# Kernel tuning notes

Measured on AMD Instinct MI355X. Metric: run time of the kernel, lower is better.

## Reference

```python
import jax, jax.numpy as jnp
import numpy as np

HIDDEN = 64
INPUT = 19


def _lstm_layer(x, Wih, Whh, bih, bhh):
    # x: [B, T, I]; Wih: [4H, I]; Whh: [4H, H]; biases: [4H]
    B, T, _ = x.shape
    H = Whh.shape[1]
    # Input contribution for all timesteps at once (big GEMM).
    zx = jnp.einsum('bti,gi->btg', x, Wih) + bih + bhh  # [B, T, 4H]

    def step(carry, z_t):
        h, c = carry
        z = z_t + h @ Whh.T  # [B, 4H]
        i, f, g, o = jnp.split(z, 4, axis=-1)  # torch gate order: i, f, g, o
        i = jax.nn.sigmoid(i)
        f = jax.nn.sigmoid(f)
        g = jnp.tanh(g)
        o = jax.nn.sigmoid(o)
        c = f * c + i * g
        h = o * jnp.tanh(c)
        return (h, c), h

    h0 = jnp.zeros((B, H), x.dtype)
    (_, _), hs = jax.lax.scan(step, (h0, h0), jnp.swapaxes(zx, 0, 1))
    return jnp.swapaxes(hs, 0, 1)  # [B, T, H]


def setup_inputs() -> dict:
    key = jax.random.key(0)
    ks = jax.random.split(key, 12)
    B, T = 4096, 168
    s = 1.0 / np.sqrt(HIDDEN)  # torch LSTM/Linear init scale
    u = lambda k, shape: jax.random.uniform(k, shape, jnp.float32, -s, s)
    return {
        'x': jax.random.normal(ks[0], (B, T, INPUT), jnp.float32),
        'Wih0': u(ks[1], (4 * HIDDEN, INPUT)),
        'Whh0': u(ks[2], (4 * HIDDEN, HIDDEN)),
        'bih0': u(ks[3], (4 * HIDDEN,)),
        'bhh0': u(ks[4], (4 * HIDDEN,)),
        'Wih1': u(ks[5], (4 * HIDDEN, HIDDEN)),
        'Whh1': u(ks[6], (4 * HIDDEN, HIDDEN)),
        'bih1': u(ks[7], (4 * HIDDEN,)),
        'bhh1': u(ks[8], (4 * HIDDEN,)),
        'Wfc': u(ks[9], (1, HIDDEN)),
        'bfc': u(ks[10], (1,)),
    }


def reference(x, Wih0, Whh0, bih0, bhh0, Wih1, Whh1, bih1, bhh1, Wfc, bfc):
    h1 = _lstm_layer(x, Wih0, Whh0, bih0, bhh0)   # [B, T, H]
    h2 = _lstm_layer(h1, Wih1, Whh1, bih1, bhh1)  # [B, T, H]
    out = h2[:, -1, :] @ Wfc.T + bfc              # [B, 1]
    return out.squeeze(-1)                        # [B]
```

## Files before the change

kernel.cpp:

```cpp
#include <hip/hip_runtime.h>
#include <math.h>

#define T_STEPS 168
#define INP     19
#define HID     64
#define ROWS    16
#define NTH     512
#define HSTH    72
#define XSTH    40

typedef _Float16 half8   __attribute__((ext_vector_type(8)));
typedef float    floatx4 __attribute__((ext_vector_type(4)));

__device__ __forceinline__ float fast_sigmoid(float x) {
    return __builtin_amdgcn_rcpf(1.0f + __expf(-x));
}
__device__ __forceinline__ float fast_tanh(float x) {
    return 1.0f - 2.0f * __builtin_amdgcn_rcpf(1.0f + __expf(2.0f * x));
}

__global__ __launch_bounds__(NTH) __attribute__((amdgpu_waves_per_eu(2, 2)))
void lstm2_mfma3_kernel(const float* __restrict__ x,
                        const float* __restrict__ Wih0, const float* __restrict__ Whh0,
                        const float* __restrict__ bih0, const float* __restrict__ bhh0,
                        const float* __restrict__ Wih1, const float* __restrict__ Whh1,
                        const float* __restrict__ bih1, const float* __restrict__ bhh1,
                        const float* __restrict__ Wfc,  const float* __restrict__ bfc,
                        float* __restrict__ out)
{
    __shared__ __align__(16) _Float16 xf [2][ROWS][XSTH];
    __shared__ __align__(16) _Float16 h1f[2][ROWS][HSTH];
    __shared__ __align__(16) _Float16 h2f[2][ROWS][HSTH];
    __shared__ float hout[ROWS][HID];

    const int tid  = threadIdx.x;
    const int b0   = blockIdx.x * ROWS;
    const int wv   = tid >> 6;
    const int lane = tid & 63;
    const int quad = lane >> 4;
    const int l16  = lane & 15;
    const int kq   = quad * 8;
    const int lay  = wv >> 2;
    const int uq   = wv & 3;
    const int u    = uq * 16 + l16;

    half8 bfr[4][4];
    float bz[4];
#pragma unroll
    for (int gi = 0; gi < 4; ++gi) {
        const int gr = gi * 64 + u;
        if (lay == 0) {
            const float* wr = Wih0 + gr * INP;
#pragma unroll
            for (int e = 0; e < 8; ++e) {
                const int k = kq + e;
                bfr[gi][0][e] = (k < INP) ? (_Float16)wr[k] : (_Float16)0.0f;
            }
            const float* hr = Whh0 + gr * HID;
#pragma unroll
            for (int e = 0; e < 8; ++e) {
                bfr[gi][1][e] = (_Float16)hr[kq + e];
                bfr[gi][2][e] = (_Float16)hr[32 + kq + e];
            }
            bfr[gi][3] = bfr[gi][2];
            bz[gi] = bih0[gr] + bhh0[gr];
        } else {
            const float* ir = Wih1 + gr * HID;
            const float* hr = Whh1 + gr * HID;
#pragma unroll
            for (int e = 0; e < 8; ++e) {
                bfr[gi][0][e] = (_Float16)ir[kq + e];
                bfr[gi][1][e] = (_Float16)ir[32 + kq + e];
                bfr[gi][2][e] = (_Float16)hr[kq + e];
                bfr[gi][3][e] = (_Float16)hr[32 + kq + e];
            }
            bz[gi] = bih1[gr] + bhh1[gr];
        }
    }

    float cst[4] = {0.f, 0.f, 0.f, 0.f};

    int srr = 0, sii = 0;
    const float* xsrc = nullptr;
    if (tid < ROWS * INP) {
        srr = tid / INP; sii = tid - srr * INP;
        xsrc = x + ((size_t)(b0 + srr) * T_STEPS) * INP + sii;
    }

    for (int e = tid; e < 2 * ROWS * XSTH; e += NTH) ((_Float16*)xf)[e] = (_Float16)0.f;
    for (int e = tid; e < 2 * ROWS * HSTH; e += NTH) {
        ((_Float16*)h1f)[e] = (_Float16)0.f;
        ((_Float16*)h2f)[e] = (_Float16)0.f;
    }
    __syncthreads();
    float xreg = 0.f;
    if (xsrc) {
        xf[0][srr][sii] = (_Float16)xsrc[0];
        xreg = xsrc[INP];
    }
    __syncthreads();

    for (int t = 0; t <= T_STEPS; ++t) {
        float xnew = 0.f;
        if (xsrc) {
            const int tn = (t + 2 < T_STEPS) ? (t + 2) : (T_STEPS - 1);
            xnew = xsrc[(size_t)tn * INP];
        }
        if (xsrc && (t + 1) < T_STEPS)
            xf[(t + 1) & 1][srr][sii] = (_Float16)xreg;

        const bool act = (lay == 0) ? (t < T_STEPS) : (t >= 1);
        if (act) {
            floatx4 acc[4];
#pragma unroll
            for (int gi = 0; gi < 4; ++gi)
                acc[gi] = (floatx4){bz[gi], bz[gi], bz[gi], bz[gi]};
            if (lay == 0) {
                const half8 ax = *(const half8*)&xf [t & 1][l16][kq];
                const half8 a0 = *(const half8*)&h1f[(t + 1) & 1][l16][kq];
                const half8 a1 = *(const half8*)&h1f[(t + 1) & 1][l16][32 + kq];
#pragma unroll
                for (int gi = 0; gi < 4; ++gi) {
                    acc[gi] = __builtin_amdgcn_mfma_f32_16x16x32_f16(ax, bfr[gi][0], acc[gi], 0, 0, 0);
                    acc[gi] = __builtin_amdgcn_mfma_f32_16x16x32_f16(a0, bfr[gi][1], acc[gi], 0, 0, 0);
                    acc[gi] = __builtin_amdgcn_mfma_f32_16x16x32_f16(a1, bfr[gi][2], acc[gi], 0, 0, 0);
                }
            } else {
                const half8 p0 = *(const half8*)&h1f[(t + 1) & 1][l16][kq];
                const half8 p1 = *(const half8*)&h1f[(t + 1) & 1][l16][32 + kq];
                const half8 q0 = *(const half8*)&h2f[t & 1][l16][kq];
                const half8 q1 = *(const half8*)&h2f[t & 1][l16][32 + kq];
#pragma unroll
                for (int gi = 0; gi < 4; ++gi) {
                    acc[gi] = __builtin_amdgcn_mfma_f32_16x16x32_f16(p0, bfr[gi][0], acc[gi], 0, 0, 0);
                    acc[gi] = __builtin_amdgcn_mfma_f32_16x16x32_f16(p1, bfr[gi][1], acc[gi], 0, 0, 0);
                    acc[gi] = __builtin_amdgcn_mfma_f32_16x16x32_f16(q0, bfr[gi][2], acc[gi], 0, 0, 0);
                    acc[gi] = __builtin_amdgcn_mfma_f32_16x16x32_f16(q1, bfr[gi][3], acc[gi], 0, 0, 0);
                }
            }
#pragma unroll
            for (int rg = 0; rg < 4; ++rg) {
                const float ig = fast_sigmoid(acc[0][rg]);
                const float fg = fast_sigmoid(acc[1][rg]);
                const float gg = fast_tanh(acc[2][rg]);
                const float og = fast_sigmoid(acc[3][rg]);
                cst[rg] = fg * cst[rg] + ig * gg;
                const float hv = og * fast_tanh(cst[rg]);
                const int row = quad * 4 + rg;
                if (lay == 0) {
                    h1f[t & 1][row][u] = (_Float16)hv;
                } else {
                    h2f[(t + 1) & 1][row][u] = (_Float16)hv;
                    if (t == T_STEPS) hout[row][u] = hv;
                }
            }
        }
        xreg = xnew;
        __syncthreads();
    }

    if (tid < ROWS) {
        float a = bfc[0];
        const float* hr = hout[tid];
#pragma unroll
        for (int k = 0; k < HID; ++k)
            a = fmaf(hr[k], Wfc[k], a);
        out[b0 + tid] = a;
    }
}

extern "C" void kernel_launch(void* const* d_in, const int* in_sizes, int n_in,
                              void* d_out, int out_size, void* d_ws, size_t ws_size,
                              hipStream_t stream) {
    const float* x    = (const float*)d_in[0];
    const float* Wih0 = (const float*)d_in[1];
    const float* Whh0 = (const float*)d_in[2];
    const float* bih0 = (const float*)d_in[3];
    const float* bhh0 = (const float*)d_in[4];
    const float* Wih1 = (const float*)d_in[5];
    const float* Whh1 = (const float*)d_in[6];
    const float* bih1 = (const float*)d_in[7];
    const float* bhh1 = (const float*)d_in[8];
    const float* Wfc  = (const float*)d_in[9];
    const float* bfc  = (const float*)d_in[10];
    float* out = (float*)d_out;

    const int B = in_sizes[0] / (T_STEPS * INP);
    const int grid = B / ROWS;

    lstm2_mfma3_kernel<<<dim3(grid), dim3(NTH), 0, stream>>>(
        x, Wih0, Whh0, bih0, bhh0, Wih1, Whh1, bih1, bhh1, Wfc, bfc, out);
}
```

Baseline: 254.5 us.

## Double waves per block to split gate activations and fold exp scaling into weights

```diff
diff --git a/kernel.cpp b/kernel.cpp
--- a/kernel.cpp
+++ b/kernel.cpp
@@ -5,22 +5,28 @@
 #define INP     19
 #define HID     64
 #define ROWS    16
-#define NTH     512
+#define NTH     1024
 #define HSTH    72
 #define XSTH    40
 
 typedef _Float16 half8   __attribute__((ext_vector_type(8)));
 typedef float    floatx4 __attribute__((ext_vector_type(4)));
 
-__device__ __forceinline__ float fast_sigmoid(float x) {
-    return __builtin_amdgcn_rcpf(1.0f + __expf(-x));
-}
-__device__ __forceinline__ float fast_tanh(float x) {
-    return 1.0f - 2.0f * __builtin_amdgcn_rcpf(1.0f + __expf(2.0f * x));
-}
-
-__global__ __launch_bounds__(NTH) __attribute__((amdgpu_waves_per_eu(2, 2)))
-void lstm2_mfma3_kernel(const float* __restrict__ x,
+#define KSIG  (-1.4426950408889634f)
+#define KTANH ( 2.8853900817779268f)
+
+__device__ __forceinline__ float exp2_hw(float x) {
+    float r; asm("v_exp_f32 %0, %1" : "=v"(r) : "v"(x)); return r;
+}
+__device__ __forceinline__ float sig_pre(float a) {
+    return __builtin_amdgcn_rcpf(1.0f + exp2_hw(a));
+}
+__device__ __forceinline__ float tanh_pre(float a) {
+    return 1.0f - 2.0f * __builtin_amdgcn_rcpf(1.0f + exp2_hw(a));
+}
+
+__global__ __launch_bounds__(NTH) __attribute__((amdgpu_waves_per_eu(4, 4)))
+void lstm2_mfma4_kernel(const float* __restrict__ x,
                         const float* __restrict__ Wih0, const float* __restrict__ Whh0,
                         const float* __restrict__ bih0, const float* __restrict__ bhh0,
                         const float* __restrict__ Wih1, const float* __restrict__ Whh1,
@@ -40,7 +46,8 @@
     const int quad = lane >> 4;
     const int l16  = lane & 15;
     const int kq   = quad * 8;
-    const int lay  = wv >> 2;
+    const int lay  = wv >> 3;
+    const int sub  = (wv >> 2) & 1;
     const int uq   = wv & 3;
     const int u    = uq * 16 + l16;
 
@@ -48,37 +55,38 @@
     float bz[4];
 #pragma unroll
     for (int gi = 0; gi < 4; ++gi) {
+        const float sc = (gi == 2) ? KTANH : KSIG;
         const int gr = gi * 64 + u;
         if (lay == 0) {
             const float* wr = Wih0 + gr * INP;
 #pragma unroll
             for (int e = 0; e < 8; ++e) {
                 const int k = kq + e;
-                bfr[gi][0][e] = (k < INP) ? (_Float16)wr[k] : (_Float16)0.0f;
+                bfr[gi][0][e] = (k < INP) ? (_Float16)(wr[k] * sc) : (_Float16)0.0f;
             }
             const float* hr = Whh0 + gr * HID;
 #pragma unroll
             for (int e = 0; e < 8; ++e) {
-                bfr[gi][1][e] = (_Float16)hr[kq + e];
-                bfr[gi][2][e] = (_Float16)hr[32 + kq + e];
+                bfr[gi][1][e] = (_Float16)(hr[kq + e] * sc);
+                bfr[gi][2][e] = (_Float16)(hr[32 + kq + e] * sc);
             }
             bfr[gi][3] = bfr[gi][2];
-            bz[gi] = bih0[gr] + bhh0[gr];
+            bz[gi] = (bih0[gr] + bhh0[gr]) * sc;
         } else {
             const float* ir = Wih1 + gr * HID;
             const float* hr = Whh1 + gr * HID;
 #pragma unroll
             for (int e = 0; e < 8; ++e) {
-                bfr[gi][0][e] = (_Float16)ir[kq + e];
-                bfr[gi][1][e] = (_Float16)ir[32 + kq + e];
-                bfr[gi][2][e] = (_Float16)hr[kq + e];
-                bfr[gi][3][e] = (_Float16)hr[32 + kq + e];
-            }
-            bz[gi] = bih1[gr] + bhh1[gr];
+                bfr[gi][0][e] = (_Float16)(ir[kq + e] * sc);
+                bfr[gi][1][e] = (_Float16)(ir[32 + kq + e] * sc);
+                bfr[gi][2][e] = (_Float16)(hr[kq + e] * sc);
+                bfr[gi][3][e] = (_Float16)(hr[32 + kq + e] * sc);
+            }
+            bz[gi] = (bih1[gr] + bhh1[gr]) * sc;
         }
     }
 
-    float cst[4] = {0.f, 0.f, 0.f, 0.f};
+    float cst[2] = {0.f, 0.f};
 
     int srr = 0, sii = 0;
     const float* xsrc = nullptr;
@@ -139,14 +147,15 @@
                 }
             }
 #pragma unroll
-            for (int rg = 0; rg < 4; ++rg) {
-                const float ig = fast_sigmoid(acc[0][rg]);
-                const float fg = fast_sigmoid(acc[1][rg]);
-                const float gg = fast_tanh(acc[2][rg]);
-                const float og = fast_sigmoid(acc[3][rg]);
+            for (int rg = 0; rg < 2; ++rg) {
+                const int ai = sub * 2 + rg;
+                const float ig = sig_pre (acc[0][ai]);
+                const float fg = sig_pre (acc[1][ai]);
+                const float gg = tanh_pre(acc[2][ai]);
+                const float og = sig_pre (acc[3][ai]);
                 cst[rg] = fg * cst[rg] + ig * gg;
-                const float hv = og * fast_tanh(cst[rg]);
-                const int row = quad * 4 + rg;
+                const float hv = og * tanh_pre(KTANH * cst[rg]);
+                const int row = quad * 4 + ai;
                 if (lay == 0) {
                     h1f[t & 1][row][u] = (_Float16)hv;
                 } else {
@@ -188,6 +197,6 @@
     const int B = in_sizes[0] / (T_STEPS * INP);
     const int grid = B / ROWS;
 
-    lstm2_mfma3_kernel<<<dim3(grid), dim3(NTH), 0, stream>>>(
+    lstm2_mfma4_kernel<<<dim3(grid), dim3(NTH), 0, stream>>>(
         x, Wih0, Whh0, bih0, bhh0, Wih1, Whh1, bih1, bhh1, Wfc, bfc, out);
 }
```

Result: slower. 302.0 us (+18.7%).
